# Optimization experiments

Hardware: AMD Instinct MI355X
Metric: run time of the kernel (lower is better)

Reference implementation:

```python
import jax, jax.numpy as jnp
import numpy as np

B, D, S = 128, 256, 512
K, H, NCLS = 50, 256, 2
THRES = 0.3  # conceptshap threshold


def _l2norm(x, axis):
    n = jnp.sqrt(jnp.sum(x * x, axis=axis, keepdims=True))
    return x / jnp.maximum(n, 1e-12)


def setup_inputs() -> dict:
    key = jax.random.key(0)
    ks = jax.random.split(key, 6)
    return {
        "f_input": jax.random.normal(ks[0], (B, D, S), dtype=jnp.float32),
        "targets": jax.random.uniform(ks[1], (B,), dtype=jnp.float32),
        "topic_vector": jax.random.uniform(ks[2], (D, K), minval=-0.5, maxval=0.5, dtype=jnp.float32),
        "rec_vector_1": jax.random.uniform(ks[3], (K, H), minval=-0.5, maxval=0.5, dtype=jnp.float32),
        "rec_vector_2": jax.random.uniform(ks[4], (H, D), minval=-0.5, maxval=0.5, dtype=jnp.float32),
        "Wc": jax.random.normal(ks[5], (D, NCLS), dtype=jnp.float32) * 0.05,
        "bc": jnp.zeros((NCLS,), dtype=jnp.float32),
        "causal": 0,
    }


def reference(f_input, targets, topic_vector, rec_vector_1, rec_vector_2, Wc, bc, causal):
    # text path (n=3), model_name != 'transformer' -> swap to [B, S, D]
    x = jnp.swapaxes(f_input, 1, 2)                # [B, S, D]
    x_n = _l2norm(x, axis=-1)                      # F.normalize(dim=n-1)
    tv_n = _l2norm(topic_vector, axis=0)           # [D, K], column-normalized

    topic_prob = jnp.einsum('bsd,dk->bsk', x, tv_n)      # [B, S, K]
    topic_prob_n = jnp.einsum('bsd,dk->bsk', x_n, tv_n)  # [B, S, K]

    # conceptshap: no softmax, hard threshold mask
    mask = (topic_prob_n > THRES).astype(topic_prob.dtype)
    topic_prob_am = topic_prob * mask
    topic_prob_sum = jnp.sum(topic_prob_am, axis=-1, keepdims=True) + 0.001
    topic_prob_nn = topic_prob_am / (topic_prob_sum + 1e-8)

    rec_layer_1 = jax.nn.relu(jnp.einsum('bsk,kh->bsh', topic_prob_nn, rec_vector_1))
    rec_layer_2 = jnp.einsum('bsh,hd->bsd', rec_layer_1, rec_vector_2)  # [B, S, D]

    ae_loss = jnp.mean((x_n - rec_layer_2) ** 2)

    rec_out = jnp.swapaxes(rec_layer_2, 1, 2)      # back to [B, D, S]
    # frozen classifier: mean over seq + linear head
    pred = jnp.mean(rec_out, axis=-1) @ Wc + bc    # [B, NCLS]

    # concept_sim: mean of per-concept top-(B//4) similarity scores, negated
    res = topic_prob_n.reshape(-1, K).T            # [K, B*S]
    topv, _ = jax.lax.top_k(res, B // 4)
    concept_sim = -jnp.mean(topv)

    concept_far = jnp.mean(tv_n.T @ tv_n - jnp.eye(K, dtype=tv_n.dtype))

    return (pred, jnp.float32(0.0), concept_sim, concept_far, topic_prob_nn, ae_loss)
```

## Files before the change

kernel.cpp:

```cpp
#include <hip/hip_runtime.h>
#include <math.h>

#define BB 128
#define DD 256
#define SS 512
#define KK 50
#define HH 256
#define TS 128
#define NTILES (BB * SS / TS)
#define NBLK (NTILES * 2)
#define BS (BB * SS)

#define CHUNK 1024
#define NCH (BS / CHUNK)
#define NCHBLK (KK * NCH / 4)
#define TOPK 32
#define MAXSURV 512
#define NSUB (TS / 16)

#define TVN_OFF 0
#define TVNT_OFF (TVN_OFF + DD * KK)
#define TPNT_OFF (TVNT_OFF + KK * DD)
#define PREDACC_OFF (TPNT_OFF + KK * BS)
#define AE_OFF (PREDACC_OFF + BB * DD)
#define SIM_OFF (AE_OFF + 1)
#define CNT_OFF (AE_OFF + 2)
#define SIMD_OFF (AE_OFF + 3)
#define TFLAG_OFF (AE_OFF + 4)
#define TCNT_OFF (TFLAG_OFF + NTILES)
#define NZERO (BB * DD + 4 + 2 * NTILES)
#define LIST_OFF (TCNT_OFF + NTILES)
#define CAND_OFF (LIST_OFF + MAXSURV)

#define OUT_NN_OFF 259
#define OUT_AE_IDX (OUT_NN_OFF + KK * BS)

__device__ __forceinline__ unsigned fkey(float f) {
  unsigned u = __float_as_uint(f);
  return (u & 0x80000000u) ? ~u : (u | 0x80000000u);
}
__device__ __forceinline__ float keyval(unsigned T) {
  unsigned u = (T & 0x80000000u) ? (T & 0x7FFFFFFFu) : ~T;
  return __uint_as_float(u);
}

__global__ __launch_bounds__(256) void tvn_kernel(const float* __restrict__ tv,
                                                  float* __restrict__ tvn,
                                                  float* __restrict__ tvnT,
                                                  float* __restrict__ zbase) {
  __shared__ float red[256];
  const int k = blockIdx.x, t = threadIdx.x;
  {
    const int gid = k * 256 + t;
    for (int i = gid; i < NZERO; i += KK * 256) zbase[i] = 0.0f;
  }
  float v = tv[t * KK + k];
  red[t] = v * v;
  __syncthreads();
  for (int off = 128; off > 0; off >>= 1) {
    if (t < off) red[t] += red[t + off];
    __syncthreads();
  }
  float inv = 1.0f / fmaxf(sqrtf(red[0]), 1e-12f);
  const float nv = v * inv;
  tvn[t * KK + k] = nv;
  tvnT[k * DD + t] = nv;
}

__global__ __launch_bounds__(256, 4) void main_kernel(
    const float* __restrict__ f_input, const float* __restrict__ tvnT,
    float* __restrict__ out_nn, float* __restrict__ tpn_t,
    float* __restrict__ ae_acc, int* __restrict__ surv_cnt,
    int* __restrict__ surv_list, int* __restrict__ tile_flag,
    int* __restrict__ tile_cnt) {
  __shared__ int wflag[4];
  __shared__ int decision;

  const int blk = blockIdx.x;
  const int tile = blk >> 1;
  const int half = blk & 1;
  const int b = tile >> 2;
  const int s0 = (tile & 3) * TS;
  const int t = threadIdx.x;
  const int lane = t & 63;
  const int wid = t >> 6;
  const int kb = __builtin_amdgcn_readfirstlane(half * 4 + wid);

  const float* tvk[7];
  bool kval[7];
  #pragma unroll
  for (int j = 0; j < 7; ++j) {
    const int k = kb + 8 * j;
    kval[j] = (k < KK);
    tvk[j] = tvnT + (size_t)(kval[j] ? k : (KK - 1)) * DD;
  }

  const float* xp = f_input + (size_t)b * DD * SS + s0 + 2 * lane;

  float acc0[7], acc1[7];
  #pragma unroll
  for (int j = 0; j < 7; ++j) { acc0[j] = 0.0f; acc1[j] = 0.0f; }

  float2 xb[2][8];
  #pragma unroll
  for (int i = 0; i < 8; ++i) xb[0][i] = *(const float2*)(xp + (size_t)i * SS);

  float s2_0 = 0.0f, s2_1 = 0.0f;
  int buf = 0;
  for (int part = 0; part < 8; ++part) {
    float p0 = 0.0f, p1 = 0.0f;
    #pragma unroll
    for (int dd = 0; dd < 32; dd += 8) {
      const int d0 = part * 32 + dd;
      const int dn = (d0 + 8 < DD) ? (d0 + 8) : 0;
      #pragma unroll
      for (int i = 0; i < 8; ++i) xb[buf ^ 1][i] = *(const float2*)(xp + (size_t)(dn + i) * SS);
      #pragma unroll
      for (int g = 0; g < 2; ++g) {
        const float2 xa = xb[buf][4 * g + 0], xc2 = xb[buf][4 * g + 1],
                     xc3 = xb[buf][4 * g + 2], xc4 = xb[buf][4 * g + 3];
        p0 += xa.x * xa.x; p0 += xc2.x * xc2.x; p0 += xc3.x * xc3.x; p0 += xc4.x * xc4.x;
        p1 += xa.y * xa.y; p1 += xc2.y * xc2.y; p1 += xc3.y * xc3.y; p1 += xc4.y * xc4.y;
        #pragma unroll
        for (int j = 0; j < 7; ++j) {
          const float4 tq = *(const float4*)(tvk[j] + d0 + 4 * g);
          acc0[j] += xa.x * tq.x; acc0[j] += xc2.x * tq.y;
          acc0[j] += xc3.x * tq.z; acc0[j] += xc4.x * tq.w;
          acc1[j] += xa.y * tq.x; acc1[j] += xc2.y * tq.y;
          acc1[j] += xc3.y * tq.z; acc1[j] += xc4.y * tq.w;
        }
      }
      buf ^= 1;
    }
    s2_0 = (part == 0) ? p0 : (s2_0 + p0);
    s2_1 = (part == 0) ? p1 : (s2_1 + p1);
  }
  const float i0 = 1.0f / fmaxf(sqrtf(s2_0), 1e-12f);
  const float i1 = 1.0f / fmaxf(sqrtf(s2_1), 1e-12f);

  bool m = false;
  const size_t gs = (size_t)b * SS + s0 + 2 * lane;
  #pragma unroll
  for (int j = 0; j < 7; ++j) {
    if (kval[j]) {
      const int k = kb + 8 * j;
      float2 o;
      o.x = acc0[j] * i0;
      o.y = acc1[j] * i1;
      *(float2*)(tpn_t + (size_t)k * BS + gs) = o;
      m = m | (o.x > 0.3f) | (o.y > 0.3f);
    }
  }

  const int w = __any((int)m);
  if (lane == 0) wflag[wid] = w;
  __syncthreads();
  const int blockAny = wflag[0] | wflag[1] | wflag[2] | wflag[3];

  if (t == 0) {
    const int old = atomicOr(&tile_flag[tile], blockAny);
    const int done = atomicAdd(&tile_cnt[tile], 1);
    int dec = 0;
    if (done == 1) {
      const int fl = old | blockAny;
      if (fl) {
        const int idx = atomicAdd(surv_cnt, 1);
        if (idx < MAXSURV) surv_list[idx] = tile;
      } else {
        atomicAdd(ae_acc, (float)TS);
        dec = 1;
      }
    }
    decision = dec;
  }
  __syncthreads();
  if (decision) {
    float* ob = out_nn + ((size_t)b * SS + s0) * KK;
    for (int p2 = t; p2 < TS * KK; p2 += 256) ob[p2] = 0.0f;
  }
}

__global__ __launch_bounds__(256) void chunk_surv_kernel(
    const float* __restrict__ tpn_t, float* __restrict__ cand,
    const float* __restrict__ f_input, const float* __restrict__ rec1,
    const float* __restrict__ rec2, const int* __restrict__ surv_cnt,
    const int* __restrict__ surv_list, float* __restrict__ out_nn,
    float* __restrict__ predacc, float* __restrict__ ae_acc) {
  __shared__ __align__(16) float NNk[KK * 20];
  __shared__ __align__(16) float R1t[HH * 20];
  __shared__ float nprt[16][17];
  __shared__ float nrm[16], invn[16];
  __shared__ float pm[8 * DD];
  __shared__ float red4[4];

  const int t = threadIdx.x;
  const int lane = t & 63, wid = t >> 6;

  if (blockIdx.x < NCHBLK) {
    const int gchunk = blockIdx.x * 4 + wid;
    const int k = gchunk >> 6;
    const int c = gchunk & (NCH - 1);
    const float* row = tpn_t + (size_t)k * BS + c * CHUNK;

    float v[16];
    unsigned key[16];
    #pragma unroll
    for (int j = 0; j < 16; ++j) {
      v[j] = row[lane + j * 64];
      key[j] = fkey(v[j]);
    }
    unsigned T = 0;
    for (int bit = 31; bit >= 0; --bit) {
      const unsigned ct = T | (1u << bit);
      int cnt = 0;
      #pragma unroll
      for (int j = 0; j < 16; ++j) cnt += (key[j] >= ct) ? 1 : 0;
      #pragma unroll
      for (int off = 1; off < 64; off <<= 1) cnt += __shfl_xor(cnt, off);
      if (cnt >= TOPK) T = ct;
    }
    int cg = 0;
    #pragma unroll
    for (int j = 0; j < 16; ++j) cg += (key[j] > T) ? 1 : 0;
    int incl = cg;
    #pragma unroll
    for (int off = 1; off < 64; off <<= 1) {
      int y = __shfl_up(incl, off);
      if (lane >= off) incl += y;
    }
    const int excl = incl - cg;
    const int total_gt = __shfl(incl, 63);

    float* cb = cand + (size_t)gchunk * TOPK;
    int pos = excl;
    #pragma unroll
    for (int j = 0; j < 16; ++j) {
      if (key[j] > T) cb[pos++] = v[j];
    }
    if (lane < TOPK - total_gt) cb[total_gt + lane] = keyval(T);
    return;
  }

  const int bid = blockIdx.x - NCHBLK;
  int cnt = *surv_cnt;
  if (cnt > MAXSURV) cnt = MAXSURV;
  const int ntask = NSUB * cnt;

  for (int task = bid; task < ntask; task += 64) {
    const int tile = surv_list[task / NSUB];
    const int q = task % NSUB;
    const int b = tile >> 2;
    const int s0 = (tile & 3) * TS + q * 16;
    const float* fb = f_input + (size_t)b * DD * SS;
    const size_t gs0 = (size_t)b * SS + s0;

    for (int p = t; p < KK * 16; p += 256) {
      const int k = p >> 4, ss = p & 15;
      NNk[k * 20 + ss] = tpn_t[(size_t)k * BS + gs0 + ss];
    }
    {
      const int ss = t & 15, part = t >> 4;
      const float* xc = fb + (size_t)(part * 16) * SS + s0 + ss;
      float p = 0.0f;
      #pragma unroll
      for (int i = 0; i < 16; ++i) {
        const float v = xc[(size_t)i * SS];
        p += v * v;
      }
      nprt[part][ss] = p;
    }
    __syncthreads();
    if (t < 16) {
      float s2 = 0.0f;
      #pragma unroll
      for (int i = 0; i < 16; ++i) s2 += nprt[i][t];
      const float n = fmaxf(sqrtf(s2), 1e-12f);
      nrm[t] = n;
      invn[t] = 1.0f / n;
      float sm = 0.0f;
      for (int k = 0; k < KK; ++k) {
        const float tpn = NNk[k * 20 + t];
        sm += (tpn > 0.3f) ? tpn * n : 0.0f;
      }
      const float idv = 1.0f / (sm + 0.001f + 1e-8f);
      for (int k = 0; k < KK; ++k) {
        const float tpn = NNk[k * 20 + t];
        NNk[k * 20 + t] = (tpn > 0.3f) ? tpn * n * idv : 0.0f;
      }
    }
    __syncthreads();

    for (int p = t; p < 16 * KK; p += 256) {
      const int ss = p / KK, k = p - ss * KK;
      out_nn[(gs0 + ss) * KK + k] = NNk[k * 20 + ss];
    }

    {
      float a[16];
      #pragma unroll
      for (int i = 0; i < 16; ++i) a[i] = 0.0f;
      #pragma unroll 2
      for (int k = 0; k < KK; ++k) {
        const float r = rec1[k * HH + t];
        const float4* np = (const float4*)&NNk[k * 20];
        #pragma unroll
        for (int qq = 0; qq < 4; ++qq) {
          const float4 nv = np[qq];
          a[qq * 4 + 0] += nv.x * r;
          a[qq * 4 + 1] += nv.y * r;
          a[qq * 4 + 2] += nv.z * r;
          a[qq * 4 + 3] += nv.w * r;
        }
      }
      #pragma unroll
      for (int i = 0; i < 16; ++i) R1t[t * 20 + i] = fmaxf(a[i], 0.0f);
    }
    __syncthreads();

    const int tx = t & 31, ty = t >> 5;
    const int d0 = tx * 8, sb = ty * 2;
    float c2[2][8];
    #pragma unroll
    for (int i = 0; i < 2; ++i)
      #pragma unroll
      for (int j = 0; j < 8; ++j) c2[i][j] = 0.0f;
    for (int h0 = 0; h0 < HH; h0 += 8) {
      float4 B0[8], B1[8];
      #pragma unroll
      for (int u = 0; u < 8; ++u) {
        B0[u] = *(const float4*)(rec2 + (h0 + u) * DD + d0);
        B1[u] = *(const float4*)(rec2 + (h0 + u) * DD + d0 + 4);
      }
      #pragma unroll
      for (int u = 0; u < 8; ++u) {
        const float2 a01 = *(const float2*)(&R1t[(h0 + u) * 20 + sb]);
        const float bv[8] = {B0[u].x, B0[u].y, B0[u].z, B0[u].w,
                             B1[u].x, B1[u].y, B1[u].z, B1[u].w};
        #pragma unroll
        for (int j = 0; j < 8; ++j) {
          c2[0][j] += a01.x * bv[j];
          c2[1][j] += a01.y * bv[j];
        }
      }
    }
    #pragma unroll
    for (int j = 0; j < 8; ++j) pm[ty * DD + d0 + j] = c2[0][j] + c2[1][j];
    __syncthreads();
    {
      float sum = 0.0f;
      #pragma unroll
      for (int r = 0; r < 8; ++r) sum += pm[r * DD + t];
      atomicAdd(&predacc[(size_t)b * DD + t], sum);
    }
    float e = 0.0f;
    #pragma unroll
    for (int j = 0; j < 8; ++j) {
      #pragma unroll
      for (int i = 0; i < 2; ++i) {
        const float x = fb[(size_t)(d0 + j) * SS + s0 + sb + i];
        const float diff = x * invn[sb + i] - c2[i][j];
        e += diff * diff;
      }
    }
    #pragma unroll
    for (int off = 1; off < 64; off <<= 1) e += __shfl_xor(e, off);
    if (lane == 0) red4[wid] = e;
    __syncthreads();
    if (t == 0) atomicAdd(ae_acc, red4[0] + red4[1] + red4[2] + red4[3]);
    __syncthreads();
  }
}

__global__ __launch_bounds__(256) void merge_finalize_kernel(
    const float* __restrict__ cand, const float* __restrict__ predacc,
    const float* __restrict__ Wc, const float* __restrict__ bc,
    const float* __restrict__ ae_acc, float* __restrict__ sim_acc,
    unsigned* __restrict__ sim_done, const float* __restrict__ tvn,
    float* __restrict__ out) {
  __shared__ float r0[256], r1[256];
  const int blk = blockIdx.x;
  const int t = threadIdx.x;

  if (blk >= BB) {
    if (t < 64) {
      const int k = blk - BB;
      const int lane = t;
      const float* row = cand + (size_t)k * (NCH * TOPK);
      float v[32];
      unsigned key[32];
      #pragma unroll
      for (int j = 0; j < 32; ++j) {
        v[j] = row[lane + j * 64];
        key[j] = fkey(v[j]);
      }
      unsigned T = 0;
      for (int bit = 31; bit >= 0; --bit) {
        const unsigned ct = T | (1u << bit);
        int cnt = 0;
        #pragma unroll
        for (int j = 0; j < 32; ++j) cnt += (key[j] >= ct) ? 1 : 0;
        #pragma unroll
        for (int off = 1; off < 64; off <<= 1) cnt += __shfl_xor(cnt, off);
        if (cnt >= TOPK) T = ct;
      }
      float s = 0.0f;
      int cgt = 0;
      #pragma unroll
      for (int j = 0; j < 32; ++j) {
        if (key[j] > T) { s += v[j]; cgt++; }
      }
      #pragma unroll
      for (int off = 1; off < 64; off <<= 1) {
        s += __shfl_xor(s, off);
        cgt += __shfl_xor(cgt, off);
      }
      if (lane == 0) {
        atomicAdd(sim_acc, s + (float)(TOPK - cgt) * keyval(T));
        __threadfence();
        const unsigned c = atomicAdd(sim_done, 1u);
        if (c == KK - 1) {
          __threadfence();
          const float tot = atomicAdd(sim_acc, 0.0f);
          out[257] = -tot * (1.0f / (float)(KK * TOPK));
        }
      }
    }
    return;
  }

  const float s = predacc[(size_t)blk * DD + t];
  r0[t] = s * Wc[t * 2 + 0];
  r1[t] = s * Wc[t * 2 + 1];
  __syncthreads();
  for (int off = 128; off > 0; off >>= 1) {
    if (t < off) { r0[t] += r0[t + off]; r1[t] += r1[t + off]; }
    __syncthreads();
  }
  if (t == 0) {
    out[blk * 2 + 0] = r0[0] * (1.0f / (float)SS) + bc[0];
    out[blk * 2 + 1] = r1[0] * (1.0f / (float)SS) + bc[1];
    if (blk == 0) {
      out[256] = 0.0f;
      out[OUT_AE_IDX] = (*ae_acc) * (1.0f / ((float)BB * (float)SS * (float)DD));
    }
  }
  if (blk == 0) {
    __syncthreads();
    float rs = 0.0f;
    for (int k = 0; k < KK; ++k) rs += tvn[t * KK + k];
    r0[t] = rs * rs;
    __syncthreads();
    for (int off = 128; off > 0; off >>= 1) {
      if (t < off) r0[t] += r0[t + off];
      __syncthreads();
    }
    if (t == 0) out[258] = (r0[0] - (float)KK) / ((float)KK * (float)KK);
  }
}

extern "C" void kernel_launch(void* const* d_in, const int* in_sizes, int n_in,
                              void* d_out, int out_size, void* d_ws, size_t ws_size,
                              hipStream_t stream) {
  (void)in_sizes; (void)n_in; (void)out_size; (void)ws_size;
  const float* f_input = (const float*)d_in[0];
  const float* tv = (const float*)d_in[2];
  const float* rec1 = (const float*)d_in[3];
  const float* rec2 = (const float*)d_in[4];
  const float* Wc = (const float*)d_in[5];
  const float* bc = (const float*)d_in[6];

  float* out = (float*)d_out;
  float* ws = (float*)d_ws;
  float* tvn = ws + TVN_OFF;
  float* tvnT = ws + TVNT_OFF;
  float* tpn_t = ws + TPNT_OFF;
  float* predacc = ws + PREDACC_OFF;
  float* ae_acc = ws + AE_OFF;
  float* sim_acc = ws + SIM_OFF;
  int* surv_cnt = (int*)(ws + CNT_OFF);
  unsigned* sim_done = (unsigned*)(ws + SIMD_OFF);
  int* tile_flag = (int*)(ws + TFLAG_OFF);
  int* tile_cnt = (int*)(ws + TCNT_OFF);
  int* surv_list = (int*)(ws + LIST_OFF);
  float* cand = ws + CAND_OFF;

  tvn_kernel<<<KK, 256, 0, stream>>>(tv, tvn, tvnT, predacc);
  main_kernel<<<NBLK, 256, 0, stream>>>(f_input, tvnT, out + OUT_NN_OFF, tpn_t,
                                        ae_acc, surv_cnt, surv_list,
                                        tile_flag, tile_cnt);
  chunk_surv_kernel<<<NCHBLK + 64, 256, 0, stream>>>(
      tpn_t, cand, f_input, rec1, rec2, surv_cnt, surv_list,
      out + OUT_NN_OFF, predacc, ae_acc);
  merge_finalize_kernel<<<BB + KK, 256, 0, stream>>>(
      cand, predacc, Wc, bc, ae_acc, sim_acc, sim_done, tvn, out);
}
```

Measured before the change: 214.3 us.

## Fuse merge/finalize into chunk kernel via last-block-done atomic counters

Result: slower. 301.2 us (+40.5%).

```diff
diff --git a/kernel.cpp b/kernel.cpp
--- a/kernel.cpp
+++ b/kernel.cpp
@@ -28,8 +28,10 @@
 #define SIMD_OFF (AE_OFF + 3)
 #define TFLAG_OFF (AE_OFF + 4)
 #define TCNT_OFF (TFLAG_OFF + NTILES)
-#define NZERO (BB * DD + 4 + 2 * NTILES)
-#define LIST_OFF (TCNT_OFF + NTILES)
+#define KDONE_OFF (TCNT_OFF + NTILES)
+#define SDONE_OFF (KDONE_OFF + KK)
+#define NZERO (BB * DD + 4 + 2 * NTILES + KK + 1)
+#define LIST_OFF (SDONE_OFF + 1)
 #define CAND_OFF (LIST_OFF + MAXSURV)
 
 #define OUT_NN_OFF 259
@@ -185,13 +187,18 @@
     const float* __restrict__ f_input, const float* __restrict__ rec1,
     const float* __restrict__ rec2, const int* __restrict__ surv_cnt,
     const int* __restrict__ surv_list, float* __restrict__ out_nn,
-    float* __restrict__ predacc, float* __restrict__ ae_acc) {
+    float* __restrict__ predacc, float* __restrict__ ae_acc,
+    int* __restrict__ kdone, int* __restrict__ sdone,
+    float* __restrict__ sim_acc, unsigned* __restrict__ sim_done,
+    const float* __restrict__ tvn, const float* __restrict__ Wc,
+    const float* __restrict__ bc, float* __restrict__ out) {
   __shared__ __align__(16) float NNk[KK * 20];
   __shared__ __align__(16) float R1t[HH * 20];
   __shared__ float nprt[16][17];
   __shared__ float nrm[16], invn[16];
   __shared__ float pm[8 * DD];
   __shared__ float red4[4];
+  __shared__ int doFin;
 
   const int t = threadIdx.x;
   const int lane = t & 63, wid = t >> 6;
@@ -238,6 +245,59 @@
       if (key[j] > T) cb[pos++] = v[j];
     }
     if (lane < TOPK - total_gt) cb[total_gt + lane] = keyval(T);
+
+    const int kc = blockIdx.x >> 4;
+    __syncthreads();
+    __threadfence();
+    if (t == 0) {
+      const int old = atomicAdd(&kdone[kc], 1);
+      doFin = (old == 15);
+    }
+    __syncthreads();
+    if (doFin) {
+      __threadfence();
+      if (t < 64) {
+        const float* mrow = cand + (size_t)kc * (NCH * TOPK);
+        float mv[32];
+        unsigned mkey[32];
+        #pragma unroll
+        for (int j = 0; j < 32; ++j) {
+          mv[j] = mrow[t + j * 64];
+          mkey[j] = fkey(mv[j]);
+        }
+        unsigned MT = 0;
+        for (int bit = 31; bit >= 0; --bit) {
+          const unsigned ct = MT | (1u << bit);
+          int cnt = 0;
+          #pragma unroll
+          for (int j = 0; j < 32; ++j) cnt += (mkey[j] >= ct) ? 1 : 0;
+          #pragma unroll
+          for (int off = 1; off < 64; off <<= 1) cnt += __shfl_xor(cnt, off);
+          if (cnt >= TOPK) MT = ct;
+        }
+        float s = 0.0f;
+        int cgt = 0;
+        #pragma unroll
+        for (int j = 0; j < 32; ++j) {
+          if (mkey[j] > MT) { s += mv[j]; cgt++; }
+        }
+        #pragma unroll
+        for (int off = 1; off < 64; off <<= 1) {
+          s += __shfl_xor(s, off);
+          cgt += __shfl_xor(cgt, off);
+        }
+        if (t == 0) {
+          atomicAdd(sim_acc, s + (float)(TOPK - cgt) * keyval(MT));
+          __threadfence();
+          const unsigned c2 = atomicAdd(sim_done, 1u);
+          if (c2 == KK - 1) {
+            __threadfence();
+            const float tot = atomicAdd(sim_acc, 0.0f);
+            out[257] = -tot * (1.0f / (float)(KK * TOPK));
+          }
+        }
+      }
+    }
     return;
   }
 
@@ -369,92 +429,65 @@
     if (t == 0) atomicAdd(ae_acc, red4[0] + red4[1] + red4[2] + red4[3]);
     __syncthreads();
   }
-}
-
-__global__ __launch_bounds__(256) void merge_finalize_kernel(
-    const float* __restrict__ cand, const float* __restrict__ predacc,
-    const float* __restrict__ Wc, const float* __restrict__ bc,
-    const float* __restrict__ ae_acc, float* __restrict__ sim_acc,
-    unsigned* __restrict__ sim_done, const float* __restrict__ tvn,
-    float* __restrict__ out) {
-  __shared__ float r0[256], r1[256];
-  const int blk = blockIdx.x;
-  const int t = threadIdx.x;
-
-  if (blk >= BB) {
-    if (t < 64) {
-      const int k = blk - BB;
-      const int lane = t;
-      const float* row = cand + (size_t)k * (NCH * TOPK);
-      float v[32];
-      unsigned key[32];
-      #pragma unroll
-      for (int j = 0; j < 32; ++j) {
-        v[j] = row[lane + j * 64];
-        key[j] = fkey(v[j]);
-      }
-      unsigned T = 0;
-      for (int bit = 31; bit >= 0; --bit) {
-        const unsigned ct = T | (1u << bit);
-        int cnt = 0;
-        #pragma unroll
-        for (int j = 0; j < 32; ++j) cnt += (key[j] >= ct) ? 1 : 0;
-        #pragma unroll
-        for (int off = 1; off < 64; off <<= 1) cnt += __shfl_xor(cnt, off);
-        if (cnt >= TOPK) T = ct;
-      }
-      float s = 0.0f;
-      int cgt = 0;
-      #pragma unroll
-      for (int j = 0; j < 32; ++j) {
-        if (key[j] > T) { s += v[j]; cgt++; }
-      }
-      #pragma unroll
-      for (int off = 1; off < 64; off <<= 1) {
-        s += __shfl_xor(s, off);
-        cgt += __shfl_xor(cgt, off);
+
+  __syncthreads();
+  __threadfence();
+  if (t == 0) {
+    const int old = atomicAdd(sdone, 1);
+    doFin = (old == 63);
+  }
+  __syncthreads();
+  if (!doFin) return;
+  __threadfence();
+
+  {
+    float2 wv[4];
+    #pragma unroll
+    for (int i = 0; i < 4; ++i) wv[i] = *(const float2*)&Wc[(lane + 64 * i) * 2];
+    const float bc0 = bc[0], bc1 = bc[1];
+    for (int i = 0; i < 32; ++i) {
+      const int b = wid * 32 + i;
+      const float* pa = predacc + (size_t)b * DD;
+      const float sv0 = pa[lane], sv1 = pa[lane + 64],
+                  sv2 = pa[lane + 128], sv3 = pa[lane + 192];
+      float a0, a1;
+      {
+#pragma clang fp contract(off)
+        const float m00 = sv0 * wv[0].x, m10 = sv1 * wv[1].x,
+                    m20 = sv2 * wv[2].x, m30 = sv3 * wv[3].x;
+        const float m01 = sv0 * wv[0].y, m11 = sv1 * wv[1].y,
+                    m21 = sv2 * wv[2].y, m31 = sv3 * wv[3].y;
+        a0 = (m00 + m20) + (m10 + m30);
+        a1 = (m01 + m21) + (m11 + m31);
+      }
+      #pragma unroll
+      for (int off = 32; off > 0; off >>= 1) {
+        a0 += __shfl_down(a0, off);
+        a1 += __shfl_down(a1, off);
       }
       if (lane == 0) {
-        atomicAdd(sim_acc, s + (float)(TOPK - cgt) * keyval(T));
-        __threadfence();
-        const unsigned c = atomicAdd(sim_done, 1u);
-        if (c == KK - 1) {
-          __threadfence();
-          const float tot = atomicAdd(sim_acc, 0.0f);
-          out[257] = -tot * (1.0f / (float)(KK * TOPK));
-        }
-      }
-    }
-    return;
-  }
-
-  const float s = predacc[(size_t)blk * DD + t];
-  r0[t] = s * Wc[t * 2 + 0];
-  r1[t] = s * Wc[t * 2 + 1];
+        out[b * 2 + 0] = a0 * (1.0f / (float)SS) + bc0;
+        out[b * 2 + 1] = a1 * (1.0f / (float)SS) + bc1;
+      }
+    }
+  }
   __syncthreads();
-  for (int off = 128; off > 0; off >>= 1) {
-    if (t < off) { r0[t] += r0[t + off]; r1[t] += r1[t + off]; }
-    __syncthreads();
-  }
-  if (t == 0) {
-    out[blk * 2 + 0] = r0[0] * (1.0f / (float)SS) + bc[0];
-    out[blk * 2 + 1] = r1[0] * (1.0f / (float)SS) + bc[1];
-    if (blk == 0) {
-      out[256] = 0.0f;
-      out[OUT_AE_IDX] = (*ae_acc) * (1.0f / ((float)BB * (float)SS * (float)DD));
-    }
-  }
-  if (blk == 0) {
-    __syncthreads();
+
+  {
     float rs = 0.0f;
     for (int k = 0; k < KK; ++k) rs += tvn[t * KK + k];
-    r0[t] = rs * rs;
+    pm[t] = rs * rs;
     __syncthreads();
     for (int off = 128; off > 0; off >>= 1) {
-      if (t < off) r0[t] += r0[t + off];
+      if (t < off) pm[t] += pm[t + off];
       __syncthreads();
     }
-    if (t == 0) out[258] = (r0[0] - (float)KK) / ((float)KK * (float)KK);
+    if (t == 0) {
+      out[258] = (pm[0] - (float)KK) / ((float)KK * (float)KK);
+      out[256] = 0.0f;
+      const float ae = atomicAdd(ae_acc, 0.0f);
+      out[OUT_AE_IDX] = ae * (1.0f / ((float)BB * (float)SS * (float)DD));
+    }
   }
 }
 
@@ -481,6 +514,8 @@
   unsigned* sim_done = (unsigned*)(ws + SIMD_OFF);
   int* tile_flag = (int*)(ws + TFLAG_OFF);
   int* tile_cnt = (int*)(ws + TCNT_OFF);
+  int* kdone = (int*)(ws + KDONE_OFF);
+  int* sdone = (int*)(ws + SDONE_OFF);
   int* surv_list = (int*)(ws + LIST_OFF);
   float* cand = ws + CAND_OFF;
 
@@ -490,7 +525,6 @@
                                         tile_flag, tile_cnt);
   chunk_surv_kernel<<<NCHBLK + 64, 256, 0, stream>>>(
       tpn_t, cand, f_input, rec1, rec2, surv_cnt, surv_list,
-      out + OUT_NN_OFF, predacc, ae_acc);
-  merge_finalize_kernel<<<BB + KK, 256, 0, stream>>>(
-      cand, predacc, Wc, bc, ae_acc, sim_acc, sim_done, tvn, out);
+      out + OUT_NN_OFF, predacc, ae_acc, kdone, sdone, sim_acc, sim_done,
+      tvn, Wc, bc, out);
 }
```
